# Optimization experiments

Hardware: AMD Instinct MI355X
Metric: run time of the kernel (lower is better)

## Reference

```python
import jax, jax.numpy as jnp
import numpy as np

D_IN = 768
D_OUT = 768
NUM_HEADS = 12
HEAD_DIM = D_OUT // NUM_HEADS


def setup_inputs() -> dict:
    key = jax.random.key(0)
    ks = jax.random.split(key, 6)
    s = 1.0 / np.sqrt(D_IN)
    X = jax.random.normal(ks[0], (4, 2048, D_IN), dtype=jnp.float32)
    Wq = jax.random.uniform(ks[1], (D_IN, D_OUT), jnp.float32, -s, s)
    Wk = jax.random.uniform(ks[2], (D_IN, D_OUT), jnp.float32, -s, s)
    Wv = jax.random.uniform(ks[3], (D_IN, D_OUT), jnp.float32, -s, s)
    Wo = jax.random.uniform(ks[4], (D_OUT, D_OUT), jnp.float32, -s, s)
    bo = jax.random.uniform(ks[5], (D_OUT,), jnp.float32, -s, s)
    return {"X": X, "Wq": Wq, "Wk": Wk, "Wv": Wv, "Wo": Wo, "bo": bo}


def reference(X, Wq, Wk, Wv, Wo, bo):
    b, n, _ = X.shape
    # QKV projections, split heads -> [b, h, n, d]
    def split(t):
        return t.reshape(b, n, NUM_HEADS, HEAD_DIM).transpose(0, 2, 1, 3)
    q = split(X @ Wq)
    k = split(X @ Wk)
    v = split(X @ Wv)
    scores = jnp.einsum('bhqd,bhkd->bhqk', q, k) / np.sqrt(HEAD_DIM).astype(np.float32)
    causal = jnp.triu(jnp.ones((n, n), dtype=bool), k=1)
    scores = jnp.where(causal, -jnp.inf, scores)
    attn = jax.nn.softmax(scores, axis=-1)  # dropout p=0 -> identity
    ctx = jnp.einsum('bhqk,bhkd->bhqd', attn, v)
    ctx = ctx.transpose(0, 2, 1, 3).reshape(b, n, D_OUT)
    return ctx @ Wo + bo
```

## Files before the change

### kernel.cpp

```cpp
#include <hip/hip_runtime.h>
#include <stdint.h>

#define B_  4
#define N_  2048
#define D_  768
#define H_  12
#define HD_ 64
#define M_  (B_*N_)

typedef short bf8 __attribute__((ext_vector_type(8)));
typedef float f32x4 __attribute__((ext_vector_type(4)));

static __device__ __forceinline__ unsigned short f2bf(float f) {
    unsigned u = __float_as_uint(f);
    unsigned r = u + 0x7fffu + ((u >> 16) & 1u);
    return (unsigned short)(r >> 16);
}

static __device__ __forceinline__ unsigned pk2bf(float f0, float f1) {
    return ((__float_as_uint(f1) + 0x8000u) & 0xFFFF0000u) |
           ((__float_as_uint(f0) + 0x8000u) >> 16);
}

#if __has_builtin(__builtin_amdgcn_exp2f)
#define EXP2(x) __builtin_amdgcn_exp2f(x)
#else
#define EXP2(x) exp2f(x)
#endif

#define GLOAD_LDS16(gptr, lptr)                                                   \
    __builtin_amdgcn_global_load_lds(                                             \
        (const __attribute__((address_space(1))) void*)(gptr),                    \
        (__attribute__((address_space(3))) void*)(lptr), 16, 0, 0)

#define QSCALE 0.1803368801111204f

__global__ __launch_bounds__(256) void prep(
    const float* __restrict__ X,
    const float* __restrict__ Wq, const float* __restrict__ Wk,
    const float* __restrict__ Wv, const float* __restrict__ Wo,
    unsigned short* __restrict__ Xb,
    unsigned short* __restrict__ Wqt, unsigned short* __restrict__ Wkt,
    unsigned short* __restrict__ Wvt, unsigned short* __restrict__ Wot)
{
    __shared__ float tile[32][33];
    const int bid = blockIdx.x;
    if (bid < 3072) {
        const size_t i = ((size_t)bid * 256 + threadIdx.x) * 8;
        const float4 a = *(const float4*)(X + i);
        const float4 b = *(const float4*)(X + i + 4);
        ushort4 lo, hi;
        lo.x = f2bf(a.x); lo.y = f2bf(a.y); lo.z = f2bf(a.z); lo.w = f2bf(a.w);
        hi.x = f2bf(b.x); hi.y = f2bf(b.y); hi.z = f2bf(b.z); hi.w = f2bf(b.w);
        *(ushort4*)(Xb + i)     = lo;
        *(ushort4*)(Xb + i + 4) = hi;
    } else {
        const int r = bid - 3072;
        const int z = r / 576;
        const int rem = r % 576;
        const float* W = (z == 0) ? Wq : (z == 1) ? Wk : (z == 2) ? Wv : Wo;
        unsigned short* Wt = (z == 0) ? Wqt : (z == 1) ? Wkt : (z == 2) ? Wvt : Wot;
        const int k0 = (rem % 24) * 32, n0 = (rem / 24) * 32;
        const int tx = threadIdx.x & 31, ty = threadIdx.x >> 5;
        #pragma unroll
        for (int i = 0; i < 4; ++i)
            tile[ty + 8 * i][tx] = W[(size_t)(k0 + ty + 8 * i) * D_ + n0 + tx];
        __syncthreads();
        #pragma unroll
        for (int i = 0; i < 4; ++i)
            Wt[(size_t)(n0 + ty + 8 * i) * D_ + k0 + tx] = f2bf(tile[tx][ty + 8 * i]);
    }
}

__global__ __launch_bounds__(512) void qkv_mfma(
    const unsigned short* __restrict__ Xb,
    const unsigned short* __restrict__ Wqt, const unsigned short* __restrict__ Wkt,
    const unsigned short* __restrict__ Wvt,
    unsigned short* __restrict__ Qb, unsigned short* __restrict__ Kb,
    unsigned short* __restrict__ Vt)
{
    __shared__ unsigned short As[2][8192];
    __shared__ unsigned short Bs[2][8192];

    const int t = threadIdx.x;
    const int wave = t >> 6, lane = t & 63;
    const int col = lane & 15, quad = lane >> 4;
    const int wm = (wave & 1) * 64;
    const int wn = (wave >> 1) * 32;

    const int orig = blockIdx.x;
    const int wgid = (orig & 7) * 144 + (orig >> 3);
    const int m0  = (wgid / 18) * 128;
    const int nm  = wgid % 18;
    const int mat = nm / 6;
    const int n0  = (nm % 6) * 128;
    const unsigned short* Wt = (mat == 0) ? Wqt : (mat == 1) ? Wkt : Wvt;
    const bool sw = (mat != 2);

    const unsigned short* Ag = Xb + (size_t)(m0 + (t >> 2)) * D_ + (t & 3) * 8;
    const unsigned short* Bg = Wt + (size_t)(n0 + (t >> 2)) * D_ + (t & 3) * 8;

#define QKV_STAGE(bsel, kk)                                                       \
    do {                                                                          \
        GLOAD_LDS16(Ag + (kk),      &As[bsel][0] + t * 8);                        \
        GLOAD_LDS16(Ag + (kk) + 32, &As[bsel][0] + 4096 + t * 8);                 \
        GLOAD_LDS16(Bg + (kk),      &Bs[bsel][0] + t * 8);                        \
        GLOAD_LDS16(Bg + (kk) + 32, &Bs[bsel][0] + 4096 + t * 8);                 \
    } while (0)

    f32x4 acc[4][2] = {};

    QKV_STAGE(0, 0);
    asm volatile("s_waitcnt vmcnt(0)" ::: "memory");
    __builtin_amdgcn_s_barrier();
    __builtin_amdgcn_sched_barrier(0);

    #pragma unroll 2
    for (int it = 0; it < 12; ++it) {
        const int cur = it & 1;
        if (it + 1 < 12) QKV_STAGE(cur ^ 1, (it + 1) * 64);

        const unsigned short* Ab = &As[cur][0];
        const unsigned short* Bb = &Bs[cur][0];
        #pragma unroll
        for (int ks = 0; ks < 2; ++ks) {
            bf8 a[4], b[2];
            #pragma unroll
            for (int i = 0; i < 4; ++i)
                a[i] = *(const bf8*)(Ab + ks * 4096 + (wm + i * 16 + col) * 32 + quad * 8);
            #pragma unroll
            for (int j = 0; j < 2; ++j)
                b[j] = *(const bf8*)(Bb + ks * 4096 + (wn + j * 16 + col) * 32 + quad * 8);
            if (sw) {
                #pragma unroll
                for (int i = 0; i < 4; ++i)
                    #pragma unroll
                    for (int j = 0; j < 2; ++j)
                        acc[i][j] = __builtin_amdgcn_mfma_f32_16x16x32_bf16(b[j], a[i], acc[i][j], 0, 0, 0);
            } else {
                #pragma unroll
                for (int i = 0; i < 4; ++i)
                    #pragma unroll
                    for (int j = 0; j < 2; ++j)
                        acc[i][j] = __builtin_amdgcn_mfma_f32_16x16x32_bf16(a[i], b[j], acc[i][j], 0, 0, 0);
            }
        }

        asm volatile("s_waitcnt vmcnt(0)" ::: "memory");
        __builtin_amdgcn_s_barrier();
        __builtin_amdgcn_sched_barrier(0);
    }
#undef QKV_STAGE

    if (sw) {
        unsigned short* Out = (mat == 0) ? Qb : Kb;
        const float qsc = (mat == 0) ? QSCALE : 1.0f;
        #pragma unroll
        for (int i = 0; i < 4; ++i) {
            const int token = m0 + wm + i * 16 + col;
            const int bb = token >> 11, nn = token & (N_ - 1);
            #pragma unroll
            for (int j = 0; j < 2; ++j) {
                const int n = n0 + wn + j * 16 + quad * 4;
                const int h = n >> 6, d = n & 63;
                ushort4 pk;
                pk.x = f2bf(acc[i][j][0] * qsc);
                pk.y = f2bf(acc[i][j][1] * qsc);
                pk.z = f2bf(acc[i][j][2] * qsc);
                pk.w = f2bf(acc[i][j][3] * qsc);
                *(ushort4*)(Out + ((size_t)(bb * H_ + h) * N_ + nn) * HD_ + d) = pk;
            }
        }
    } else {
        #pragma unroll
        for (int j = 0; j < 2; ++j) {
            const int n = n0 + wn + j * 16 + col;
            const int h = n >> 6, d = n & 63;
            #pragma unroll
            for (int i = 0; i < 4; ++i) {
                const int mb = m0 + wm + i * 16 + quad * 4;
                const int bb = mb >> 11;
                const int nn = mb & (N_ - 1);
                const int nnp = (nn & ~31) | ((quad >> 1) << 4) | ((quad & 1) << 3) |
                                ((i & 1) << 2);
                ushort4 pk;
                pk.x = f2bf(acc[i][j][0]); pk.y = f2bf(acc[i][j][1]);
                pk.z = f2bf(acc[i][j][2]); pk.w = f2bf(acc[i][j][3]);
                *(ushort4*)(Vt + ((size_t)(bb * H_ + h) * HD_ + d) * N_ + nnp) = pk;
            }
        }
    }
}

static __device__ __forceinline__ void qk_mfma8(
    const bf8 (&ka)[4][2], bf8 qb0, bf8 qb1, f32x4 (&s)[4])
{
    __builtin_amdgcn_s_setprio(1);
    #pragma unroll
    for (int kc = 0; kc < 4; ++kc) {
        s[kc] = __builtin_amdgcn_mfma_f32_16x16x32_bf16(ka[kc][0], qb0, s[kc], 0, 0, 0);
        s[kc] = __builtin_amdgcn_mfma_f32_16x16x32_bf16(ka[kc][1], qb1, s[kc], 0, 0, 0);
    }
    __builtin_amdgcn_s_setprio(0);
}

static __device__ __forceinline__ void softmax_pack(
    const f32x4 (&s)[4], int k0, int q, bool mask, float& lpart,
    bf8& pb0, bf8& pb1, int quad)
{
    float p[4][4];
    if (mask) {
        #pragma unroll
        for (int kc = 0; kc < 4; ++kc)
            #pragma unroll
            for (int r = 0; r < 4; ++r) {
                const int key = k0 + kc * 16 + quad * 4 + r;
                p[kc][r] = EXP2((key > q) ? -INFINITY : s[kc][r]);
            }
    } else {
        #pragma unroll
        for (int kc = 0; kc < 4; ++kc)
            #pragma unroll
            for (int r = 0; r < 4; ++r) p[kc][r] = EXP2(s[kc][r]);
    }

    #pragma unroll
    for (int kc = 0; kc < 4; ++kc)
        #pragma unroll
        for (int r = 0; r < 4; ++r) lpart += p[kc][r];

    uint4 u0, u1;
    u0.x = pk2bf(p[0][0], p[0][1]); u0.y = pk2bf(p[0][2], p[0][3]);
    u0.z = pk2bf(p[1][0], p[1][1]); u0.w = pk2bf(p[1][2], p[1][3]);
    u1.x = pk2bf(p[2][0], p[2][1]); u1.y = pk2bf(p[2][2], p[2][3]);
    u1.z = pk2bf(p[3][0], p[3][1]); u1.w = pk2bf(p[3][2], p[3][3]);
    pb0 = *(bf8*)&u0;
    pb1 = *(bf8*)&u1;
}

static __device__ __forceinline__ void pv_acc(
    bf8 pb0, bf8 pb1, const bf8 (&va)[4][2], f32x4 (&o)[4])
{
    __builtin_amdgcn_s_setprio(1);
    #pragma unroll
    for (int dc = 0; dc < 4; ++dc) {
        o[dc] = __builtin_amdgcn_mfma_f32_16x16x32_bf16(va[dc][0], pb0, o[dc], 0, 0, 0);
        o[dc] = __builtin_amdgcn_mfma_f32_16x16x32_bf16(va[dc][1], pb1, o[dc], 0, 0, 0);
    }
    __builtin_amdgcn_s_setprio(0);
}

__global__ __launch_bounds__(256, 3) void attn_mfma(
    const unsigned short* __restrict__ Qb,
    const unsigned short* __restrict__ Kb,
    const unsigned short* __restrict__ Vt,
    unsigned short* __restrict__ Ctxb)
{
    __shared__ unsigned short Kl[2][64 * 64];
    __shared__ unsigned short Vl[2][64 * 64];

    const int t = threadIdx.x;
    const int wave = t >> 6;
    const int lane = t & 63;
    const int col  = lane & 15;
    const int quad = lane >> 4;

    const int orig = blockIdx.x;
    const int bid  = (orig & 7) * 96 + (orig >> 3);
    const int bh  = bid >> 4;
    const int x   = bid & 15;
    const int tl  = x, th = 31 - x;
    const int q0L = tl * 64 + wave * 16;
    const int q0H = th * 64 + wave * 16;
    const int qL  = q0L + col;
    const int qH  = q0H + col;

    const unsigned short* Kp = Kb + (size_t)bh * N_ * HD_;
    const unsigned short* Vp = Vt + (size_t)bh * HD_ * N_;
    const unsigned short* QpL = Qb + ((size_t)bh * N_ + q0L) * HD_;
    const unsigned short* QpH = Qb + ((size_t)bh * N_ + q0H) * HD_;

    const bf8 qbL0 = *(const bf8*)(QpL + (size_t)col * HD_ + quad * 8);
    const bf8 qbL1 = *(const bf8*)(QpL + (size_t)col * HD_ + 32 + quad * 8);
    const bf8 qbH0 = *(const bf8*)(QpH + (size_t)col * HD_ + quad * 8);
    const bf8 qbH1 = *(const bf8*)(QpH + (size_t)col * HD_ + 32 + quad * 8);

    f32x4 oL[4] = {}, oH[4] = {};
    float lL = 0.f, lH = 0.f;

    const int srow = t >> 3;
    const int gcol = (t & 7) ^ (srow & 7);
    const unsigned short* Kg = Kp + (size_t)srow * HD_ + gcol * 8;
    const unsigned short* Vg = Vp + (size_t)srow * N_ + gcol * 8;
    unsigned short* KlD = &Kl[0][0] + t * 8;
    unsigned short* VlD = &Vl[0][0] + t * 8;

#define ATT_STAGE(bsel, kt_)                                                       \
    do {                                                                           \
        GLOAD_LDS16(Kg + (size_t)(kt_) * 64 * HD_,        KlD + (bsel) * 4096);    \
        GLOAD_LDS16(Kg + (size_t)((kt_) * 64 + 32) * HD_, KlD + (bsel) * 4096 + 2048); \
        GLOAD_LDS16(Vg + (kt_) * 64,                      VlD + (bsel) * 4096);    \
        GLOAD_LDS16(Vg + (size_t)32 * N_ + (kt_) * 64,    VlD + (bsel) * 4096 + 2048); \
    } while (0)

    const int iters = 32 - x;

    const int rd0 = ((quad    ) ^ (col & 7)) * 8;
    const int rd1 = ((quad + 4) ^ (col & 7)) * 8;

    ATT_STAGE(0, 0);

    for (int kt = 0; kt < iters; ++kt) {
        const int k0 = kt * 64;
        const bool actL = (kt <= tl);
        const int cur = kt & 1;

        asm volatile("s_waitcnt vmcnt(0)" ::: "memory");
        __builtin_amdgcn_s_barrier();
        __builtin_amdgcn_sched_barrier(0);

        if (kt + 1 < iters) ATT_STAGE(cur ^ 1, kt + 1);

        const unsigned short* Kc = &Kl[cur][0];
        const unsigned short* Vc = &Vl[cur][0];

        bf8 ka[4][2];
        #pragma unroll
        for (int kc = 0; kc < 4; ++kc) {
            const unsigned short* kr = Kc + (kc * 16 + col) * 64;
            ka[kc][0] = *(const bf8*)(kr + rd0);
            ka[kc][1] = *(const bf8*)(kr + rd1);
        }
        bf8 va[4][2];
        #pragma unroll
        for (int dc = 0; dc < 4; ++dc) {
            const unsigned short* vr = Vc + (dc * 16 + col) * 64;
            va[dc][0] = *(const bf8*)(vr + rd0);
            va[dc][1] = *(const bf8*)(vr + rd1);
        }

        f32x4 sH[4] = {};
        qk_mfma8(ka, qbH0, qbH1, sH);
        f32x4 sL[4] = {};
        if (actL) qk_mfma8(ka, qbL0, qbL1, sL);

        bf8 pbH0, pbH1;
        softmax_pack(sH, k0, qH, kt == th, lH, pbH0, pbH1, quad);
        pv_acc(pbH0, pbH1, va, oH);

        if (actL) {
            bf8 pbL0, pbL1;
            softmax_pack(sL, k0, qL, kt == tl, lL, pbL0, pbL1, quad);
            pv_acc(pbL0, pbL1, va, oL);
        }
    }
#undef ATT_STAGE

    const int b = bh / H_;
    const int h = bh % H_;
    {
        float l = lH;
        l += __shfl_xor(l, 16, 64);
        l += __shfl_xor(l, 32, 64);
        const float inv = 1.0f / l;
        unsigned short* cp = Ctxb + ((size_t)(b * N_ + qH)) * D_ + h * HD_;
        #pragma unroll
        for (int dc = 0; dc < 4; ++dc) {
            uint2 pk;
            pk.x = pk2bf(oH[dc][0] * inv, oH[dc][1] * inv);
            pk.y = pk2bf(oH[dc][2] * inv, oH[dc][3] * inv);
            *(uint2*)(cp + dc * 16 + quad * 4) = pk;
        }
    }
    {
        float l = lL;
        l += __shfl_xor(l, 16, 64);
        l += __shfl_xor(l, 32, 64);
        const float inv = 1.0f / l;
        unsigned short* cp = Ctxb + ((size_t)(b * N_ + qL)) * D_ + h * HD_;
        #pragma unroll
        for (int dc = 0; dc < 4; ++dc) {
            uint2 pk;
            pk.x = pk2bf(oL[dc][0] * inv, oL[dc][1] * inv);
            pk.y = pk2bf(oL[dc][2] * inv, oL[dc][3] * inv);
            *(uint2*)(cp + dc * 16 + quad * 4) = pk;
        }
    }
}

__global__ __launch_bounds__(512) void out_mfma(
    const unsigned short* __restrict__ Ctxb,
    const unsigned short* __restrict__ Wot,
    const float* __restrict__ bo,
    float* __restrict__ Out)
{
    __shared__ unsigned short As[2][8192];
    __shared__ unsigned short Bs[2][8192];

    const int t = threadIdx.x;
    const int wave = t >> 6, lane = t & 63;
    const int col = lane & 15, quad = lane >> 4;
    const int wm = (wave & 1) * 64;
    const int wn = (wave >> 1) * 32;

    const int orig = blockIdx.x;
    const int wgid = (orig & 7) * 48 + (orig >> 3);
    const int m0 = (wgid / 6) * 128;
    const int n0 = (wgid % 6) * 128;

    const unsigned short* Ag = Ctxb + (size_t)(m0 + (t >> 2)) * D_ + (t & 3) * 8;
    const unsigned short* Bg = Wot + (size_t)(n0 + (t >> 2)) * D_ + (t & 3) * 8;

#define OUT_STAGE(bsel, kk)                                                       \
    do {                                                                          \
        GLOAD_LDS16(Ag + (kk),      &As[bsel][0] + t * 8);                        \
        GLOAD_LDS16(Ag + (kk) + 32, &As[bsel][0] + 4096 + t * 8);                 \
        GLOAD_LDS16(Bg + (kk),      &Bs[bsel][0] + t * 8);                        \
        GLOAD_LDS16(Bg + (kk) + 32, &Bs[bsel][0] + 4096 + t * 8);                 \
    } while (0)

    f32x4 acc[4][2] = {};

    OUT_STAGE(0, 0);
    asm volatile("s_waitcnt vmcnt(0)" ::: "memory");
    __builtin_amdgcn_s_barrier();
    __builtin_amdgcn_sched_barrier(0);

    #pragma unroll 2
    for (int it = 0; it < 12; ++it) {
        const int cur = it & 1;
        if (it + 1 < 12) OUT_STAGE(cur ^ 1, (it + 1) * 64);

        const unsigned short* Ab = &As[cur][0];
        const unsigned short* Bb = &Bs[cur][0];
        #pragma unroll
        for (int ks = 0; ks < 2; ++ks) {
            bf8 a[4], b[2];
            #pragma unroll
            for (int i = 0; i < 4; ++i)
                a[i] = *(const bf8*)(Ab + ks * 4096 + (wm + i * 16 + col) * 32 + quad * 8);
            #pragma unroll
            for (int j = 0; j < 2; ++j)
                b[j] = *(const bf8*)(Bb + ks * 4096 + (wn + j * 16 + col) * 32 + quad * 8);
            #pragma unroll
            for (int i = 0; i < 4; ++i)
                #pragma unroll
                for (int j = 0; j < 2; ++j)
                    acc[i][j] = __builtin_amdgcn_mfma_f32_16x16x32_bf16(b[j], a[i], acc[i][j], 0, 0, 0);
        }

        asm volatile("s_waitcnt vmcnt(0)" ::: "memory");
        __builtin_amdgcn_s_barrier();
        __builtin_amdgcn_sched_barrier(0);
    }
#undef OUT_STAGE

    #pragma unroll
    for (int i = 0; i < 4; ++i) {
        const int m = m0 + wm + i * 16 + col;
        #pragma unroll
        for (int j = 0; j < 2; ++j) {
            const int n = n0 + wn + j * 16 + quad * 4;
            const float4 bias = *(const float4*)(bo + n);
            float4 o;
            o.x = acc[i][j][0] + bias.x;
            o.y = acc[i][j][1] + bias.y;
            o.z = acc[i][j][2] + bias.z;
            o.w = acc[i][j][3] + bias.w;
            *(float4*)(Out + (size_t)m * D_ + n) = o;
        }
    }
}

extern "C" void kernel_launch(void* const* d_in, const int* in_sizes, int n_in,
                              void* d_out, int out_size, void* d_ws, size_t ws_size,
                              hipStream_t stream) {
    const float* X  = (const float*)d_in[0];
    const float* Wq = (const float*)d_in[1];
    const float* Wk = (const float*)d_in[2];
    const float* Wv = (const float*)d_in[3];
    const float* Wo = (const float*)d_in[4];
    const float* bo = (const float*)d_in[5];
    float* out = (float*)d_out;

    const size_t elems = (size_t)M_ * D_;
    const size_t welems = (size_t)D_ * D_;
    unsigned short* Xb  = (unsigned short*)d_ws;
    unsigned short* Wqt = Xb + elems;
    unsigned short* Wkt = Wqt + welems;
    unsigned short* Wvt = Wkt + welems;
    unsigned short* Wot = Wvt + welems;
    unsigned short* Qb  = Wot + welems;
    unsigned short* Kb  = Qb + elems;
    unsigned short* Vt  = Kb + elems;
    unsigned short* Ctxb = Xb;

    prep<<<dim3(3072 + 2304), 256, 0, stream>>>(X, Wq, Wk, Wv, Wo,
                                                Xb, Wqt, Wkt, Wvt, Wot);

    qkv_mfma<<<dim3(1152), 512, 0, stream>>>(Xb, Wqt, Wkt, Wvt, Qb, Kb, Vt);

    attn_mfma<<<dim3(B_ * H_ * 16), 256, 0, stream>>>(Qb, Kb, Vt, Ctxb);

    out_mfma<<<dim3(384), 512, 0, stream>>>(Ctxb, Wot, bo, out);
}
```

Baseline: 197.0 us.

## Compute Q, K, V tiles in one block to share X tile loads

Each QKV GEMM block now loads one X tile and the matching Wq, Wk and Wv tiles, and accumulates all three outputs at once. This cuts redundant global loads of X across the three projections and reduces the grid from 1152 to 384 blocks. The K step per stage shrinks from 64 to 32, which doubles the barrier count. Accumulator registers triple, so occupancy may drop, and 384 blocks may underfill the GPU.

```diff
diff --git a/kernel.cpp b/kernel.cpp
--- a/kernel.cpp
+++ b/kernel.cpp
@@ -79,8 +79,8 @@
     unsigned short* __restrict__ Qb, unsigned short* __restrict__ Kb,
     unsigned short* __restrict__ Vt)
 {
-    __shared__ unsigned short As[2][8192];
-    __shared__ unsigned short Bs[2][8192];
+    __shared__ unsigned short As[2][4096];
+    __shared__ unsigned short Bs[2][3][4096];
 
     const int t = threadIdx.x;
     const int wave = t >> 6, lane = t & 63;
@@ -89,26 +89,24 @@
     const int wn = (wave >> 1) * 32;
 
     const int orig = blockIdx.x;
-    const int wgid = (orig & 7) * 144 + (orig >> 3);
-    const int m0  = (wgid / 18) * 128;
-    const int nm  = wgid % 18;
-    const int mat = nm / 6;
-    const int n0  = (nm % 6) * 128;
-    const unsigned short* Wt = (mat == 0) ? Wqt : (mat == 1) ? Wkt : Wvt;
-    const bool sw = (mat != 2);
-
-    const unsigned short* Ag = Xb + (size_t)(m0 + (t >> 2)) * D_ + (t & 3) * 8;
-    const unsigned short* Bg = Wt + (size_t)(n0 + (t >> 2)) * D_ + (t & 3) * 8;
+    const int wgid = (orig & 7) * 48 + (orig >> 3);
+    const int m0 = (wgid / 6) * 128;
+    const int n0 = (wgid % 6) * 128;
+
+    const unsigned short* Ag = Xb  + (size_t)(m0 + (t >> 2)) * D_ + (t & 3) * 8;
+    const unsigned short* Bq = Wqt + (size_t)(n0 + (t >> 2)) * D_ + (t & 3) * 8;
+    const unsigned short* Bk = Wkt + (size_t)(n0 + (t >> 2)) * D_ + (t & 3) * 8;
+    const unsigned short* Bv = Wvt + (size_t)(n0 + (t >> 2)) * D_ + (t & 3) * 8;
 
 #define QKV_STAGE(bsel, kk)                                                       \
     do {                                                                          \
-        GLOAD_LDS16(Ag + (kk),      &As[bsel][0] + t * 8);                        \
-        GLOAD_LDS16(Ag + (kk) + 32, &As[bsel][0] + 4096 + t * 8);                 \
-        GLOAD_LDS16(Bg + (kk),      &Bs[bsel][0] + t * 8);                        \
-        GLOAD_LDS16(Bg + (kk) + 32, &Bs[bsel][0] + 4096 + t * 8);                 \
+        GLOAD_LDS16(Ag + (kk), &As[bsel][0]    + t * 8);                          \
+        GLOAD_LDS16(Bq + (kk), &Bs[bsel][0][0] + t * 8);                          \
+        GLOAD_LDS16(Bk + (kk), &Bs[bsel][1][0] + t * 8);                          \
+        GLOAD_LDS16(Bv + (kk), &Bs[bsel][2][0] + t * 8);                          \
     } while (0)
 
-    f32x4 acc[4][2] = {};
+    f32x4 accQ[4][2] = {}, accK[4][2] = {}, accV[4][2] = {};
 
     QKV_STAGE(0, 0);
     asm volatile("s_waitcnt vmcnt(0)" ::: "memory");
@@ -116,35 +114,29 @@
     __builtin_amdgcn_sched_barrier(0);
 
     #pragma unroll 2
-    for (int it = 0; it < 12; ++it) {
+    for (int it = 0; it < 24; ++it) {
         const int cur = it & 1;
-        if (it + 1 < 12) QKV_STAGE(cur ^ 1, (it + 1) * 64);
-
-        const unsigned short* Ab = &As[cur][0];
-        const unsigned short* Bb = &Bs[cur][0];
-        #pragma unroll
-        for (int ks = 0; ks < 2; ++ks) {
-            bf8 a[4], b[2];
-            #pragma unroll
-            for (int i = 0; i < 4; ++i)
-                a[i] = *(const bf8*)(Ab + ks * 4096 + (wm + i * 16 + col) * 32 + quad * 8);
-            #pragma unroll
-            for (int j = 0; j < 2; ++j)
-                b[j] = *(const bf8*)(Bb + ks * 4096 + (wn + j * 16 + col) * 32 + quad * 8);
-            if (sw) {
-                #pragma unroll
-                for (int i = 0; i < 4; ++i)
-                    #pragma unroll
-                    for (int j = 0; j < 2; ++j)
-                        acc[i][j] = __builtin_amdgcn_mfma_f32_16x16x32_bf16(b[j], a[i], acc[i][j], 0, 0, 0);
-            } else {
-                #pragma unroll
-                for (int i = 0; i < 4; ++i)
-                    #pragma unroll
-                    for (int j = 0; j < 2; ++j)
-                        acc[i][j] = __builtin_amdgcn_mfma_f32_16x16x32_bf16(a[i], b[j], acc[i][j], 0, 0, 0);
+        if (it + 1 < 24) QKV_STAGE(cur ^ 1, (it + 1) * 32);
+
+        bf8 a[4], bq[2], bk[2], bv[2];
+        #pragma unroll
+        for (int i = 0; i < 4; ++i)
+            a[i] = *(const bf8*)(&As[cur][0] + (wm + i * 16 + col) * 32 + quad * 8);
+        #pragma unroll
+        for (int j = 0; j < 2; ++j) {
+            const int off = (wn + j * 16 + col) * 32 + quad * 8;
+            bq[j] = *(const bf8*)(&Bs[cur][0][0] + off);
+            bk[j] = *(const bf8*)(&Bs[cur][1][0] + off);
+            bv[j] = *(const bf8*)(&Bs[cur][2][0] + off);
+        }
+        #pragma unroll
+        for (int i = 0; i < 4; ++i)
+            #pragma unroll
+            for (int j = 0; j < 2; ++j) {
+                accQ[i][j] = __builtin_amdgcn_mfma_f32_16x16x32_bf16(bq[j], a[i], accQ[i][j], 0, 0, 0);
+                accK[i][j] = __builtin_amdgcn_mfma_f32_16x16x32_bf16(bk[j], a[i], accK[i][j], 0, 0, 0);
+                accV[i][j] = __builtin_amdgcn_mfma_f32_16x16x32_bf16(a[i], bv[j], accV[i][j], 0, 0, 0);
             }
-        }
 
         asm volatile("s_waitcnt vmcnt(0)" ::: "memory");
         __builtin_amdgcn_s_barrier();
@@ -152,42 +144,43 @@
     }
 #undef QKV_STAGE
 
-    if (sw) {
-        unsigned short* Out = (mat == 0) ? Qb : Kb;
-        const float qsc = (mat == 0) ? QSCALE : 1.0f;
+    #pragma unroll
+    for (int i = 0; i < 4; ++i) {
+        const int token = m0 + wm + i * 16 + col;
+        const int bb = token >> 11, nn = token & (N_ - 1);
+        #pragma unroll
+        for (int j = 0; j < 2; ++j) {
+            const int n = n0 + wn + j * 16 + quad * 4;
+            const int h = n >> 6, d = n & 63;
+            const size_t base = ((size_t)(bb * H_ + h) * N_ + nn) * HD_ + d;
+            ushort4 pq;
+            pq.x = f2bf(accQ[i][j][0] * QSCALE);
+            pq.y = f2bf(accQ[i][j][1] * QSCALE);
+            pq.z = f2bf(accQ[i][j][2] * QSCALE);
+            pq.w = f2bf(accQ[i][j][3] * QSCALE);
+            *(ushort4*)(Qb + base) = pq;
+            ushort4 pk;
+            pk.x = f2bf(accK[i][j][0]); pk.y = f2bf(accK[i][j][1]);
+            pk.z = f2bf(accK[i][j][2]); pk.w = f2bf(accK[i][j][3]);
+            *(ushort4*)(Kb + base) = pk;
+        }
+    }
+
+    #pragma unroll
+    for (int j = 0; j < 2; ++j) {
+        const int n = n0 + wn + j * 16 + col;
+        const int h = n >> 6, d = n & 63;
         #pragma unroll
         for (int i = 0; i < 4; ++i) {
-            const int token = m0 + wm + i * 16 + col;
-            const int bb = token >> 11, nn = token & (N_ - 1);
-            #pragma unroll
-            for (int j = 0; j < 2; ++j) {
-                const int n = n0 + wn + j * 16 + quad * 4;
-                const int h = n >> 6, d = n & 63;
-                ushort4 pk;
-                pk.x = f2bf(acc[i][j][0] * qsc);
-                pk.y = f2bf(acc[i][j][1] * qsc);
-                pk.z = f2bf(acc[i][j][2] * qsc);
-                pk.w = f2bf(acc[i][j][3] * qsc);
-                *(ushort4*)(Out + ((size_t)(bb * H_ + h) * N_ + nn) * HD_ + d) = pk;
-            }
-        }
-    } else {
-        #pragma unroll
-        for (int j = 0; j < 2; ++j) {
-            const int n = n0 + wn + j * 16 + col;
-            const int h = n >> 6, d = n & 63;
-            #pragma unroll
-            for (int i = 0; i < 4; ++i) {
-                const int mb = m0 + wm + i * 16 + quad * 4;
-                const int bb = mb >> 11;
-                const int nn = mb & (N_ - 1);
-                const int nnp = (nn & ~31) | ((quad >> 1) << 4) | ((quad & 1) << 3) |
-                                ((i & 1) << 2);
-                ushort4 pk;
-                pk.x = f2bf(acc[i][j][0]); pk.y = f2bf(acc[i][j][1]);
-                pk.z = f2bf(acc[i][j][2]); pk.w = f2bf(acc[i][j][3]);
-                *(ushort4*)(Vt + ((size_t)(bb * H_ + h) * HD_ + d) * N_ + nnp) = pk;
-            }
+            const int mb = m0 + wm + i * 16 + quad * 4;
+            const int bb = mb >> 11;
+            const int nn = mb & (N_ - 1);
+            const int nnp = (nn & ~31) | ((quad >> 1) << 4) | ((quad & 1) << 3) |
+                            ((i & 1) << 2);
+            ushort4 pk;
+            pk.x = f2bf(accV[i][j][0]); pk.y = f2bf(accV[i][j][1]);
+            pk.z = f2bf(accV[i][j][2]); pk.w = f2bf(accV[i][j][3]);
+            *(ushort4*)(Vt + ((size_t)(bb * H_ + h) * HD_ + d) * N_ + nnp) = pk;
         }
     }
 }
@@ -498,7 +491,7 @@
     prep<<<dim3(3072 + 2304), 256, 0, stream>>>(X, Wq, Wk, Wv, Wo,
                                                 Xb, Wqt, Wkt, Wvt, Wot);
 
-    qkv_mfma<<<dim3(1152), 512, 0, stream>>>(Xb, Wqt, Wkt, Wvt, Qb, Kb, Vt);
+    qkv_mfma<<<dim3(384), 512, 0, stream>>>(Xb, Wqt, Wkt, Wvt, Qb, Kb, Vt);
 
     attn_mfma<<<dim3(B_ * H_ * 16), 256, 0, stream>>>(Qb, Kb, Vt, Ctxb);
 
```

New measurement: 207.8 us. +5.5%, slower.
